# Kernel optimization log

Hardware: AMD Instinct MI355X
Metric: run time of the kernel (lower is better)

The kernel has to match this reference:

```python
import jax, jax.numpy as jnp
import numpy as np

IN_FEATS = 128
OUT_FEATS = 128
ASSIGN_DIM = 256
BATCH_SIZE = 8
N = 12288
E = 196608
CPG = ASSIGN_DIM // BATCH_SIZE  # clusters per graph (block width of the mask)


def setup_inputs() -> dict:
    key = jax.random.key(0)
    ks = jax.random.split(key, 6)
    x = jax.random.normal(ks[0], (N, IN_FEATS), dtype=jnp.float32)
    edge_index = jax.random.randint(ks[1], (2, E), 0, N, dtype=jnp.int32)
    batch = jnp.sort(jax.random.randint(ks[2], (N,), 0, BATCH_SIZE, dtype=jnp.int32))
    s = 1.0 / np.sqrt(2 * IN_FEATS)
    W_embd = jax.random.uniform(ks[3], (2 * IN_FEATS, OUT_FEATS), minval=-s, maxval=s, dtype=jnp.float32)
    b_embd = jnp.zeros((OUT_FEATS,), jnp.float32)
    W_pool = jax.random.uniform(ks[4], (2 * IN_FEATS, ASSIGN_DIM), minval=-s, maxval=s, dtype=jnp.float32)
    b_pool = jnp.zeros((ASSIGN_DIM,), jnp.float32)
    return dict(x=x, edge_index=edge_index, batch=batch,
                W_embd=W_embd, b_embd=b_embd, W_pool=W_pool, b_pool=b_pool)


def _sage_conv(x, src, dst, W, b):
    # GraphSAGE mean aggregator, concat([self, agg]) @ W + b, row L2-normalize.
    agg = jax.ops.segment_sum(x[src], dst, num_segments=N)                 # [N, F]
    deg = jax.ops.segment_sum(jnp.ones((E,), x.dtype), dst, num_segments=N)
    agg = agg / jnp.maximum(deg, 1.0)[:, None]
    h = jnp.concatenate([x, agg], axis=-1) @ W + b
    return h / jnp.maximum(jnp.linalg.norm(h, axis=-1, keepdims=True), 1e-12)


def _masked_softmax_nonme(m, mask):
    # memory_efficient=False branch of masked_softmax
    r = jax.nn.softmax(m * mask, axis=-1)
    r = r * mask
    return r / (r.sum(axis=-1, keepdims=True) + 1e-13)


def reference(x, edge_index, batch, W_embd, b_embd, W_pool, b_pool):
    src, dst = edge_index[0], edge_index[1]
    embed = _sage_conv(x, src, dst, W_embd, b_embd)    # [N, out_feats]
    pooled = _sage_conv(x, src, dst, W_pool, b_pool)   # [N, assign_dim]

    # block-diagonal mask: node i sees the assign columns of its own graph
    col_graph = jnp.arange(ASSIGN_DIM, dtype=batch.dtype) // CPG
    mask = (batch[:, None] == col_graph[None, :]).astype(pooled.dtype)  # [N, assign_dim]

    result = _masked_softmax_nonme(pooled, mask)        # [N, assign_dim]
    h = result.T @ embed                                # [assign_dim, out_feats]

    # adjacency coarsening: S^T A S with edge weights = 1 (duplicates sum)
    Ar = jax.ops.segment_sum(result[dst], src, num_segments=N)  # A @ result
    adj_new = result.T @ Ar                              # [assign_dim, assign_dim]

    # link prediction loss: ||A_dense - S S^T||_F / N^2 (dense NxN, as original)
    A_dense = jnp.zeros((N, N), result.dtype).at[src, dst].add(1.0)
    adj_loss = jnp.linalg.norm(A_dense - result @ result.T) / (N ** 2)

    # entropy loss over Categorical(probs=mask): uniform over each block
    p = mask / mask.sum(axis=-1, keepdims=True)
    ent = -jnp.sum(jnp.where(p > 0, p * jnp.log(jnp.where(p > 0, p, 1.0)), 0.0), axis=-1)
    entropy_loss = ent.sum()

    return adj_new, h, adj_loss, entropy_loss
```

## Files before the change

### kernel.cpp

```cpp
#include <hip/hip_runtime.h>
#include <math.h>

#define NN 12288
#define EE 196608
#define FIN 128
#define AD 256
#define NG 8
#define ACH 32
#define GCH 16
#define BCAP 64
#define APITCH 8256
#define HPITCH 4160
#define GPITCH 1088

using short8 = __attribute__((ext_vector_type(8))) short;
using floatx4 = __attribute__((ext_vector_type(4))) float;

__device__ __forceinline__ unsigned short f2bf(float f) {
  union { float f; unsigned u; } v; v.f = f;
  unsigned r = v.u + 0x7FFFu + ((v.u >> 16) & 1u);
  return (unsigned short)(r >> 16);
}


__global__ __launch_bounds__(256) void k_edgeB(const int* __restrict__ src, const int* __restrict__ dst,
    const int* __restrict__ batch,
    const float* __restrict__ We, const float* __restrict__ be,
    const float* __restrict__ Wp, const float* __restrict__ bp,
    unsigned* cnt_dst, unsigned* cnt_src, int* __restrict__ bdst, int* __restrict__ bsrc,
    unsigned short* __restrict__ WTb, float* __restrict__ bcat, int* __restrict__ gstart) {
  unsigned i = blockIdx.x * 256u + threadIdx.x;
  if (i < EE) {
    int s = src[i], d = dst[i];
    unsigned p = atomicAdd(&cnt_dst[d], 1u);
    if (p < BCAP) bdst[(size_t)d * BCAP + p] = s;
  } else if (i < 2u * EE) {
    unsigned e = i - EE;
    int s = src[e], d = dst[e];
    int gd = batch[d];
    unsigned q = atomicAdd(&cnt_src[s], 1u);
    if (q < BCAP) bsrc[(size_t)s * BCAP + q] = (gd << 14) | d;
  } else {
    unsigned j = i - 2u * EE;
    {
      unsigned n = j >> 8, k = j & 255u;
      float v = (n < 128u) ? We[k * 128u + n] : Wp[k * 256u + (n - 128u)];
      WTb[j] = f2bf(v);
    }
    if (j < 384u) bcat[j] = (j < 128u) ? be[j] : bp[j - 128u];
    if (j <= NG) {
      int g = (int)j, lo = 0, hi = NN;
      while (lo < hi) { int mid = (lo + hi) >> 1; if (batch[mid] < g) lo = mid + 1; else hi = mid; }
      gstart[g] = lo;
    }
  }
}


__global__ __launch_bounds__(256) void k_dupagg(const float* __restrict__ x,
    const unsigned* __restrict__ cnt_dst, const int* __restrict__ bdst,
    unsigned short* __restrict__ Zb, unsigned* __restrict__ dup_part) {
  int node = blockIdx.x * 4 + (threadIdx.x >> 6);
  int lane = threadIdx.x & 63;
  int h = lane >> 5, c = lane & 31;
  unsigned deg = cnt_dst[node];
  unsigned m = deg < BCAP ? deg : BCAP;
  const int* bk = bdst + (size_t)node * BCAP;
  const float4* x4 = (const float4*)x;

  int si = ((unsigned)lane < m) ? bk[lane] : -2;

  unsigned cnt = 0;
  for (unsigned j = 0; j < m; j++) {
    int sj = __shfl(si, (int)j, 64);
    cnt += (si == sj) ? 1u : 0u;
  }

  float4 a = {0.f, 0.f, 0.f, 0.f};
  for (unsigned e = (unsigned)h; e < m; e += 2) {
    int sj = __shfl(si, (int)e, 64);
    float4 v = x4[(size_t)sj * 32 + c];
    a.x += v.x; a.y += v.y; a.z += v.z; a.w += v.w;
  }

  a.x += __shfl_xor(a.x, 32, 64);
  a.y += __shfl_xor(a.y, 32, 64);
  a.z += __shfl_xor(a.z, 32, 64);
  a.w += __shfl_xor(a.w, 32, 64);

#pragma unroll
  for (int o = 32; o >= 1; o >>= 1) cnt += __shfl_xor(cnt, o, 64);
  if (lane == 0) dup_part[node] = cnt;

  float inv = 1.f / fmaxf((float)deg, 1.f);
  float4 sv = x4[(size_t)node * 32 + c];
  ushort4 o4;
  if (h == 0) {
    o4.x = f2bf(sv.x); o4.y = f2bf(sv.y); o4.z = f2bf(sv.z); o4.w = f2bf(sv.w);
  } else {
    o4.x = f2bf(a.x * inv); o4.y = f2bf(a.y * inv);
    o4.z = f2bf(a.z * inv); o4.w = f2bf(a.w * inv);
  }
  ((ushort4*)Zb)[(size_t)node * 64 + h * 32 + c] = o4;
}


__global__ __launch_bounds__(256) void k_gemmnorm(const unsigned short* __restrict__ Zb,
    const unsigned short* __restrict__ WTb, const float* __restrict__ bcat,
    const int* __restrict__ batch, float* __restrict__ embed, float* __restrict__ Rc) {
  __shared__ unsigned short Bl[24 * 512];
  __shared__ unsigned short Al[4 * 512];
  int t = threadIdx.x;
  int gm = blockIdx.x * 64;
  int w = t >> 6, l = t & 63;

  floatx4 acc[24] = {};

  for (int kc = 0; kc < 8; kc++) {
    __syncthreads();
#pragma unroll
    for (int i = 0; i < 7; i++) {
      int p = t + i * 256;
      if (p < 1536) {
        int n = p >> 2, quad = p & 3;
        uint4 v = *(const uint4*)&WTb[(size_t)n * 256 + kc * 32 + quad * 8];
        *(uint4*)&Bl[(n >> 4) * 512 + ((n & 15) + 16 * quad) * 8] = v;
      } else {
        int p2 = p - 1536;
        int m = p2 >> 2, quad = p2 & 3;
        uint4 v = *(const uint4*)&Zb[(size_t)(gm + m) * 256 + kc * 32 + quad * 8];
        *(uint4*)&Al[(m >> 4) * 512 + ((m & 15) + 16 * quad) * 8] = v;
      }
    }
    __syncthreads();
    short8 a = *(const short8*)&Al[w * 512 + l * 8];
#pragma unroll
    for (int tt = 0; tt < 24; tt++) {
      short8 b = *(const short8*)&Bl[tt * 512 + l * 8];
      acc[tt] = __builtin_amdgcn_mfma_f32_16x16x32_bf16(a, b, acc[tt], 0, 0, 0);
    }
  }

  int col16 = l & 15, quad = l >> 4;
#pragma unroll
  for (int tt = 0; tt < 24; tt++) {
    float b = bcat[tt * 16 + col16];
    acc[tt][0] += b; acc[tt][1] += b; acc[tt][2] += b; acc[tt][3] += b;
  }

#pragma unroll
  for (int r = 0; r < 4; r++) {
    int node = gm + w * 16 + quad * 4 + r;
    float ss = 0.f;
#pragma unroll
    for (int tt = 0; tt < 8; tt++) { float v = acc[tt][r]; ss += v * v; }
#pragma unroll
    for (int o = 8; o >= 1; o >>= 1) ss += __shfl_xor(ss, o, 64);
    float inv = 1.f / fmaxf(sqrtf(ss), 1e-12f);
#pragma unroll
    for (int tt = 0; tt < 8; tt++)
      embed[(size_t)node * 128 + tt * 16 + col16] = acc[tt][r] * inv;
    float ss2 = 0.f;
#pragma unroll
    for (int tt = 8; tt < 24; tt++) { float v = acc[tt][r]; ss2 += v * v; }
#pragma unroll
    for (int o = 8; o >= 1; o >>= 1) ss2 += __shfl_xor(ss2, o, 64);
    float inv2 = 1.f / fmaxf(sqrtf(ss2), 1e-12f);
    int g = batch[node];
    float v0 = 0.f, v1 = 0.f;
#pragma unroll
    for (int tg = 0; tg < 8; tg++) {
      bool sel = (tg == g);
      v0 = sel ? acc[8 + 2 * tg][r] : v0;
      v1 = sel ? acc[9 + 2 * tg][r] : v1;
    }
    v0 *= inv2; v1 *= inv2;
    float mx = fmaxf(v0, v1);
#pragma unroll
    for (int o = 8; o >= 1; o >>= 1) mx = fmaxf(mx, __shfl_xor(mx, o, 64));
    float e0 = expf(v0 - mx), e1 = expf(v1 - mx);
    float sm = e0 + e1;
#pragma unroll
    for (int o = 8; o >= 1; o >>= 1) sm += __shfl_xor(sm, o, 64);
    float rr = 1.f / sm;
    Rc[(size_t)node * 32 + col16] = e0 * rr;
    Rc[(size_t)node * 32 + 16 + col16] = e1 * rr;
  }
}


__global__ __launch_bounds__(256) void k_ar(const float* __restrict__ Rc,
    const unsigned* __restrict__ cnt_src, const int* __restrict__ bsrc,
    float* __restrict__ Ar) {
  int node = blockIdx.x * 4 + (threadIdx.x >> 6);
  int lane = threadIdx.x & 63;
  int lg = lane >> 3, li = lane & 7;
  unsigned deg = cnt_src[node];
  unsigned m = deg < BCAP ? deg : BCAP;
  const int* bk = bsrc + (size_t)node * BCAP;
  const float4* R4 = (const float4*)Rc;

  int pk = ((unsigned)lane < m) ? bk[lane] : (8 << 14);

  float4 acc[8] = {};
#pragma unroll 2
  for (unsigned k = 0; k < m; k += 8) {
    int packed = __shfl(pk, (int)(k + (unsigned)lg), 64);
    int d = packed & 16383, g = packed >> 14;
    float4 r = R4[(size_t)d * 8 + li];
#pragma unroll
    for (int j = 0; j < 8; j++) {
      float wj = (g == j) ? 1.f : 0.f;
      acc[j].x = fmaf(wj, r.x, acc[j].x);
      acc[j].y = fmaf(wj, r.y, acc[j].y);
      acc[j].z = fmaf(wj, r.z, acc[j].z);
      acc[j].w = fmaf(wj, r.w, acc[j].w);
    }
  }

#pragma unroll
  for (int j = 0; j < 8; j++) {
#pragma unroll
    for (int o = 8; o <= 32; o <<= 1) {
      acc[j].x += __shfl_xor(acc[j].x, o, 64);
      acc[j].y += __shfl_xor(acc[j].y, o, 64);
      acc[j].z += __shfl_xor(acc[j].z, o, 64);
      acc[j].w += __shfl_xor(acc[j].w, o, 64);
    }
  }
  float4 wv = acc[0];
#pragma unroll
  for (int j = 1; j < 8; j++) if (lg == j) wv = acc[j];
  ((float4*)Ar)[(size_t)node * 64 + lane] = wv;
}


__global__ __launch_bounds__(256) void k_big3(const float* __restrict__ Rc,
    const float* __restrict__ embed, const float* __restrict__ Ar, const int* __restrict__ gstart,
    float* __restrict__ part_h, float* __restrict__ part_adj, float* __restrict__ Gpart) {
  int role = blockIdx.z;
  int g = blockIdx.x, ch = blockIdx.y;
  if (role == 2 && ch >= GCH) return;
  int s0 = gstart[g], e0 = gstart[g + 1];
  int nch = (role == 2) ? GCH : ACH;
  int per = (e0 - s0 + nch - 1) / nch;
  int i0 = s0 + ch * per;
  int i1 = i0 + per; if (i1 > e0) i1 = e0;
  int t = threadIdx.x;
  __shared__ float rcs[128][32];

  if (role == 0) {
    int f4 = t & 31, c1g = t >> 5;
    float4 acc[4] = {};
    const float4* E4 = (const float4*)embed;
    for (int ib = i0; ib < i1; ib += 64) {
      int cnt = i1 - ib; if (cnt > 64) cnt = 64;
      __syncthreads();
      const float4* s4 = (const float4*)(Rc + (size_t)ib * 32);
      for (int idx = t; idx < cnt * 8; idx += 256) ((float4*)rcs)[idx] = s4[idx];
      __syncthreads();
      for (int n = 0; n < cnt; n++) {
        float4 e4 = E4[(size_t)(ib + n) * 32 + f4];
        float4 r = *(const float4*)&rcs[n][c1g * 4];
        float rv[4] = {r.x, r.y, r.z, r.w};
#pragma unroll
        for (int j = 0; j < 4; j++) {
          acc[j].x += rv[j] * e4.x; acc[j].y += rv[j] * e4.y;
          acc[j].z += rv[j] * e4.z; acc[j].w += rv[j] * e4.w;
        }
      }
    }
    float* p = part_h + (size_t)(g * ACH + ch) * HPITCH;
#pragma unroll
    for (int j = 0; j < 4; j++)
      *(float4*)&p[(c1g * 4 + j) * 128 + f4 * 4] = acc[j];
  } else if (role == 1) {
    int c2q = t & 63, c1g = t >> 6;
    float4 acc[8] = {};
    const float4* Ar4 = (const float4*)Ar;
    for (int ib = i0; ib < i1; ib += 64) {
      int cnt = i1 - ib; if (cnt > 64) cnt = 64;
      __syncthreads();
      const float4* s4 = (const float4*)(Rc + (size_t)ib * 32);
      for (int idx = t; idx < cnt * 8; idx += 256) ((float4*)rcs)[idx] = s4[idx];
      __syncthreads();
      for (int n = 0; n < cnt; n++) {
        float4 a4 = Ar4[(size_t)(ib + n) * 64 + c2q];
        float4 r0 = *(const float4*)&rcs[n][c1g * 8];
        float4 r1 = *(const float4*)&rcs[n][c1g * 8 + 4];
        float rv[8] = {r0.x, r0.y, r0.z, r0.w, r1.x, r1.y, r1.z, r1.w};
#pragma unroll
        for (int j = 0; j < 8; j++) {
          acc[j].x += rv[j] * a4.x; acc[j].y += rv[j] * a4.y;
          acc[j].z += rv[j] * a4.z; acc[j].w += rv[j] * a4.w;
        }
      }
    }
    float* p = part_adj + (size_t)(g * ACH + ch) * APITCH;
#pragma unroll
    for (int j = 0; j < 8; j++)
      *(float4*)&p[(c1g * 8 + j) * 256 + c2q * 4] = acc[j];
  } else {
    int c2q = t & 7, c1 = t >> 3;
    float4 acc = {};
    for (int ib = i0; ib < i1; ib += 128) {
      int cnt = i1 - ib; if (cnt > 128) cnt = 128;
      __syncthreads();
      const float4* s4 = (const float4*)(Rc + (size_t)ib * 32);
      for (int idx = t; idx < cnt * 8; idx += 256) ((float4*)rcs)[idx] = s4[idx];
      __syncthreads();
      for (int n = 0; n < cnt; n++) {
        float4 r2 = *(const float4*)&rcs[n][c2q * 4];
        float r1 = rcs[n][c1];
        acc.x += r1 * r2.x; acc.y += r1 * r2.y; acc.z += r1 * r2.z; acc.w += r1 * r2.w;
      }
    }
    *(float4*)&Gpart[(size_t)(g * GCH + ch) * GPITCH + c1 * 32 + c2q * 4] = acc;
  }
}


__global__ __launch_bounds__(256) void k_red3(const float* __restrict__ part_adj,
    const float* __restrict__ part_h, const float* __restrict__ Gpart,
    const unsigned* __restrict__ dup_part,
    float* __restrict__ outa, float* __restrict__ outh,
    double* __restrict__ acc, unsigned* __restrict__ done, float* __restrict__ out) {
  int b = blockIdx.x, t = threadIdx.x;
  int lane = t & 63;
  if (b < 256) {
    int i = b * 256 + t;
    int g = i >> 13, off = i & 8191;
    const float* base = part_adj + (size_t)g * ACH * APITCH + off;
    float s = 0.f;
#pragma unroll
    for (int ch = 0; ch < ACH; ch++) s += base[(size_t)ch * APITCH];
    outa[i] = s;
    if (t == b) atomicAdd(&acc[0], (double)s);
  } else if (b < 384) {
    int j = (b - 256) * 256 + t;
    int g = j >> 12, off = j & 4095;
    const float* base = part_h + (size_t)g * ACH * HPITCH + off;
    float s = 0.f;
#pragma unroll
    for (int ch = 0; ch < ACH; ch++) s += base[(size_t)ch * HPITCH];
    outh[j] = s;
  } else if (b < 416) {
    int j = (b - 384) * 256 + t;
    int g = j >> 10, off = j & 1023;
    const float* base = Gpart + (size_t)g * GCH * GPITCH + off;
    float s = 0.f;
#pragma unroll
    for (int ch = 0; ch < GCH; ch++) s += base[(size_t)ch * GPITCH];
    double g2 = (double)s * (double)s;
#pragma unroll
    for (int o = 32; o >= 1; o >>= 1) g2 += __shfl_xor(g2, o, 64);
    if (lane == 0) atomicAdd(&acc[1], g2);
  } else {
    int j = (b - 416) * 256 + t;
    double a2 = (double)dup_part[j];
#pragma unroll
    for (int o = 32; o >= 1; o >>= 1) a2 += __shfl_xor(a2, o, 64);
    if (lane == 0) atomicAdd(&acc[2], a2);
  }
  __syncthreads();
  if (t == 0) {
    unsigned prev = atomicAdd(done, 1u);
    if (prev == gridDim.x - 1) {
      double trf = atomicAdd(&acc[0], 0.0);
      double g2f = atomicAdd(&acc[1], 0.0);
      double a2f = atomicAdd(&acc[2], 0.0);
      double val = a2f - 2.0 * trf + g2f;
      if (val < 0.0) val = 0.0;
      out[98304] = (float)(sqrt(val) / ((double)NN * (double)NN));
      out[98305] = (float)((double)NN * log(32.0));
    }
  }
}


extern "C" void kernel_launch(void* const* d_in, const int* in_sizes, int n_in,
                              void* d_out, int out_size, void* d_ws, size_t ws_size,
                              hipStream_t stream) {
  const float* x = (const float*)d_in[0];
  const int* ei = (const int*)d_in[1];
  const int* src = ei;
  const int* dst = ei + EE;
  const int* batch = (const int*)d_in[2];
  const float* Wemb = (const float*)d_in[3];
  const float* bemb = (const float*)d_in[4];
  const float* Wpool = (const float*)d_in[5];
  const float* bpool = (const float*)d_in[6];
  float* out = (float*)d_out;

  char* w = (char*)d_ws;
  size_t off = 0;
  auto A = [&](size_t bytes) -> char* {
    char* p = w + off;
    off += (bytes + 255) & ~(size_t)255;
    return p;
  };
  unsigned* cnt_dst = (unsigned*)A(NN * 4);
  unsigned* cnt_src = (unsigned*)A(NN * 4);
  double* acc = (double*)A(3 * 8);
  unsigned* done = (unsigned*)A(4);
  size_t zero_bytes = off;
  int* bdst = (int*)A((size_t)NN * BCAP * 4);
  int* bsrc = (int*)A((size_t)NN * BCAP * 4);
  int* gstart = (int*)A(64);
  unsigned* dup_part = (unsigned*)A(NN * 4);
  unsigned short* Zb = (unsigned short*)A((size_t)NN * 256 * 2);
  float* embed = (float*)A((size_t)NN * FIN * 4);
  float* Rc = (float*)A((size_t)NN * 32 * 4);
  float* Ar = (float*)A((size_t)NN * AD * 4);
  unsigned short* WTb = (unsigned short*)A(384 * 256 * 2);
  float* bcat = (float*)A(384 * 4);
  float* part_h = (float*)A((size_t)8 * ACH * HPITCH * 4);
  float* part_adj = (float*)A((size_t)8 * ACH * APITCH * 4);
  float* Gpart = (float*)A((size_t)8 * GCH * GPITCH * 4);
  (void)ws_size; (void)in_sizes; (void)n_in; (void)out_size;

  hipMemsetAsync(d_ws, 0, zero_bytes, stream);
  k_edgeB<<<dim3(2 * EE / 256 + 384), dim3(256), 0, stream>>>(src, dst, batch,
      Wemb, bemb, Wpool, bpool, cnt_dst, cnt_src, bdst, bsrc, WTb, bcat, gstart);
  k_dupagg<<<dim3(NN / 4), dim3(256), 0, stream>>>(x, cnt_dst, bdst, Zb, dup_part);
  k_gemmnorm<<<dim3(NN / 64), dim3(256), 0, stream>>>(Zb, WTb, bcat, batch, embed, Rc);
  k_ar<<<dim3(NN / 4), dim3(256), 0, stream>>>(Rc, cnt_src, bsrc, Ar);
  k_big3<<<dim3(8, ACH, 3), dim3(256), 0, stream>>>(Rc, embed, Ar, gstart, part_h, part_adj, Gpart);
  k_red3<<<dim3(464), dim3(256), 0, stream>>>(part_adj, part_h, Gpart, dup_part,
      out, out + 65536, acc, done, out);
}
```

Measured before the change: 169.2 us.

## Fuse adjacency gather into coarsening GEMM and accumulate adj via atomics

The kernel that computes A@R into a global NxAD buffer is removed. Its per-node gather now runs inside the adj-coarsening role of the big kernel, with each block building Ar rows for 16 nodes in shared memory and consuming them right away. Partial adj tiles are float-atomically added straight into the output, which drops the part_adj buffer and its reduction. The trace now reads the diagonal from the finished output. This avoids writing and re-reading a 12 MB Ar buffer and one launch, at the cost of float atomics (nondeterministic summation order), an extra memset, and a gather that is serialized inside fewer blocks.

Result: slower. 226.5 us (+33.8%).

```diff
diff --git a/kernel.cpp b/kernel.cpp
--- a/kernel.cpp
+++ b/kernel.cpp
@@ -9,7 +9,6 @@
 #define ACH 32
 #define GCH 16
 #define BCAP 64
-#define APITCH 8256
 #define HPITCH 4160
 #define GPITCH 1088
 
@@ -189,69 +188,96 @@
 }
 
 
-__global__ __launch_bounds__(256) void k_ar(const float* __restrict__ Rc,
+__global__ __launch_bounds__(256) void k_bigF(const float* __restrict__ Rc,
+    const float* __restrict__ embed,
     const unsigned* __restrict__ cnt_src, const int* __restrict__ bsrc,
-    float* __restrict__ Ar) {
-  int node = blockIdx.x * 4 + (threadIdx.x >> 6);
-  int lane = threadIdx.x & 63;
-  int lg = lane >> 3, li = lane & 7;
-  unsigned deg = cnt_src[node];
-  unsigned m = deg < BCAP ? deg : BCAP;
-  const int* bk = bsrc + (size_t)node * BCAP;
-  const float4* R4 = (const float4*)Rc;
-
-  int pk = ((unsigned)lane < m) ? bk[lane] : (8 << 14);
-
-  float4 acc[8] = {};
-#pragma unroll 2
-  for (unsigned k = 0; k < m; k += 8) {
-    int packed = __shfl(pk, (int)(k + (unsigned)lg), 64);
-    int d = packed & 16383, g = packed >> 14;
-    float4 r = R4[(size_t)d * 8 + li];
-#pragma unroll
-    for (int j = 0; j < 8; j++) {
-      float wj = (g == j) ? 1.f : 0.f;
-      acc[j].x = fmaf(wj, r.x, acc[j].x);
-      acc[j].y = fmaf(wj, r.y, acc[j].y);
-      acc[j].z = fmaf(wj, r.z, acc[j].z);
-      acc[j].w = fmaf(wj, r.w, acc[j].w);
-    }
-  }
-
-#pragma unroll
-  for (int j = 0; j < 8; j++) {
-#pragma unroll
-    for (int o = 8; o <= 32; o <<= 1) {
-      acc[j].x += __shfl_xor(acc[j].x, o, 64);
-      acc[j].y += __shfl_xor(acc[j].y, o, 64);
-      acc[j].z += __shfl_xor(acc[j].z, o, 64);
-      acc[j].w += __shfl_xor(acc[j].w, o, 64);
-    }
-  }
-  float4 wv = acc[0];
-#pragma unroll
-  for (int j = 1; j < 8; j++) if (lg == j) wv = acc[j];
-  ((float4*)Ar)[(size_t)node * 64 + lane] = wv;
-}
-
-
-__global__ __launch_bounds__(256) void k_big3(const float* __restrict__ Rc,
-    const float* __restrict__ embed, const float* __restrict__ Ar, const int* __restrict__ gstart,
-    float* __restrict__ part_h, float* __restrict__ part_adj, float* __restrict__ Gpart) {
+    const int* __restrict__ gstart,
+    float* __restrict__ part_h, float* __restrict__ Gpart, float* __restrict__ outa) {
   int role = blockIdx.z;
   int g = blockIdx.x, ch = blockIdx.y;
-  if (role == 2 && ch >= GCH) return;
+  int t = threadIdx.x;
+  __shared__ __align__(16) char smem[18432];
   int s0 = gstart[g], e0 = gstart[g + 1];
-  int nch = (role == 2) ? GCH : ACH;
-  int per = (e0 - s0 + nch - 1) / nch;
-  int i0 = s0 + ch * per;
-  int i1 = i0 + per; if (i1 > e0) i1 = e0;
-  int t = threadIdx.x;
-  __shared__ float rcs[128][32];
-
-  if (role == 0) {
+
+  if (role == 1) {
+    int per = (e0 - s0 + 63) >> 6;
+    int i0 = s0 + ch * per;
+    int i1 = i0 + per; if (i1 > e0) i1 = e0;
+    int w = t >> 6, lane = t & 63;
+    int lg = lane >> 3, li = lane & 7;
+    int c1g = t >> 6, c2q = t & 63;
+    float4* ar_s = (float4*)smem;
+    float* rc_s = (float*)(smem + 16384);
+    const float4* R4 = (const float4*)Rc;
+    float4 racc[8] = {};
+    for (int ib = i0; ib < i1; ib += 16) {
+      int cnt = i1 - ib; if (cnt > 16) cnt = 16;
+      __syncthreads();
+      for (int idx = t; idx < cnt * 8; idx += 256)
+        ((float4*)rc_s)[idx] = R4[(size_t)ib * 8 + idx];
+      for (int nl = w; nl < cnt; nl += 4) {
+        int node = ib + nl;
+        unsigned deg = cnt_src[node];
+        unsigned m = deg < BCAP ? deg : BCAP;
+        const int* bk = bsrc + (size_t)node * BCAP;
+        int pk = ((unsigned)lane < m) ? bk[lane] : (8 << 14);
+        float4 a8[8] = {};
+        for (unsigned k = 0; k < m; k += 8) {
+          int packed = __shfl(pk, (int)(k + (unsigned)lg), 64);
+          int d = packed & 16383, gg = packed >> 14;
+          float4 r = R4[(size_t)d * 8 + li];
+#pragma unroll
+          for (int j = 0; j < 8; j++) {
+            float wj = (gg == j) ? 1.f : 0.f;
+            a8[j].x = fmaf(wj, r.x, a8[j].x);
+            a8[j].y = fmaf(wj, r.y, a8[j].y);
+            a8[j].z = fmaf(wj, r.z, a8[j].z);
+            a8[j].w = fmaf(wj, r.w, a8[j].w);
+          }
+        }
+#pragma unroll
+        for (int j = 0; j < 8; j++) {
+#pragma unroll
+          for (int o = 8; o <= 32; o <<= 1) {
+            a8[j].x += __shfl_xor(a8[j].x, o, 64);
+            a8[j].y += __shfl_xor(a8[j].y, o, 64);
+            a8[j].z += __shfl_xor(a8[j].z, o, 64);
+            a8[j].w += __shfl_xor(a8[j].w, o, 64);
+          }
+        }
+        float4 wv = a8[0];
+#pragma unroll
+        for (int j = 1; j < 8; j++) if (lg == j) wv = a8[j];
+        ar_s[nl * 64 + lane] = wv;
+      }
+      __syncthreads();
+      for (int n = 0; n < cnt; n++) {
+        float4 a4 = ar_s[n * 64 + c2q];
+        const float* rr = &rc_s[n * 32 + c1g * 8];
+#pragma unroll
+        for (int j = 0; j < 8; j++) {
+          float rv = rr[j];
+          racc[j].x += rv * a4.x; racc[j].y += rv * a4.y;
+          racc[j].z += rv * a4.z; racc[j].w += rv * a4.w;
+        }
+      }
+    }
+#pragma unroll
+    for (int j = 0; j < 8; j++) {
+      float* dp = &outa[(size_t)(g * 32 + c1g * 8 + j) * 256 + c2q * 4];
+      atomicAdd(dp + 0, racc[j].x);
+      atomicAdd(dp + 1, racc[j].y);
+      atomicAdd(dp + 2, racc[j].z);
+      atomicAdd(dp + 3, racc[j].w);
+    }
+  } else if (role == 0) {
+    if (ch >= ACH) return;
+    int per = (e0 - s0 + ACH - 1) / ACH;
+    int i0 = s0 + ch * per;
+    int i1 = i0 + per; if (i1 > e0) i1 = e0;
+    float (*rcs)[32] = (float(*)[32])smem;
     int f4 = t & 31, c1g = t >> 5;
-    float4 acc[4] = {};
+    float4 hacc[4] = {};
     const float4* E4 = (const float4*)embed;
     for (int ib = i0; ib < i1; ib += 64) {
       int cnt = i1 - ib; if (cnt > 64) cnt = 64;
@@ -265,44 +291,23 @@
         float rv[4] = {r.x, r.y, r.z, r.w};
 #pragma unroll
         for (int j = 0; j < 4; j++) {
-          acc[j].x += rv[j] * e4.x; acc[j].y += rv[j] * e4.y;
-          acc[j].z += rv[j] * e4.z; acc[j].w += rv[j] * e4.w;
+          hacc[j].x += rv[j] * e4.x; hacc[j].y += rv[j] * e4.y;
+          hacc[j].z += rv[j] * e4.z; hacc[j].w += rv[j] * e4.w;
         }
       }
     }
     float* p = part_h + (size_t)(g * ACH + ch) * HPITCH;
 #pragma unroll
     for (int j = 0; j < 4; j++)
-      *(float4*)&p[(c1g * 4 + j) * 128 + f4 * 4] = acc[j];
-  } else if (role == 1) {
-    int c2q = t & 63, c1g = t >> 6;
-    float4 acc[8] = {};
-    const float4* Ar4 = (const float4*)Ar;
-    for (int ib = i0; ib < i1; ib += 64) {
-      int cnt = i1 - ib; if (cnt > 64) cnt = 64;
-      __syncthreads();
-      const float4* s4 = (const float4*)(Rc + (size_t)ib * 32);
-      for (int idx = t; idx < cnt * 8; idx += 256) ((float4*)rcs)[idx] = s4[idx];
-      __syncthreads();
-      for (int n = 0; n < cnt; n++) {
-        float4 a4 = Ar4[(size_t)(ib + n) * 64 + c2q];
-        float4 r0 = *(const float4*)&rcs[n][c1g * 8];
-        float4 r1 = *(const float4*)&rcs[n][c1g * 8 + 4];
-        float rv[8] = {r0.x, r0.y, r0.z, r0.w, r1.x, r1.y, r1.z, r1.w};
-#pragma unroll
-        for (int j = 0; j < 8; j++) {
-          acc[j].x += rv[j] * a4.x; acc[j].y += rv[j] * a4.y;
-          acc[j].z += rv[j] * a4.z; acc[j].w += rv[j] * a4.w;
-        }
-      }
-    }
-    float* p = part_adj + (size_t)(g * ACH + ch) * APITCH;
-#pragma unroll
-    for (int j = 0; j < 8; j++)
-      *(float4*)&p[(c1g * 8 + j) * 256 + c2q * 4] = acc[j];
+      *(float4*)&p[(c1g * 4 + j) * 128 + f4 * 4] = hacc[j];
   } else {
+    if (ch >= GCH) return;
+    int per = (e0 - s0 + GCH - 1) / GCH;
+    int i0 = s0 + ch * per;
+    int i1 = i0 + per; if (i1 > e0) i1 = e0;
+    float (*rcs)[32] = (float(*)[32])smem;
     int c2q = t & 7, c1 = t >> 3;
-    float4 acc = {};
+    float4 gacc = {};
     for (int ib = i0; ib < i1; ib += 128) {
       int cnt = i1 - ib; if (cnt > 128) cnt = 128;
       __syncthreads();
@@ -312,40 +317,35 @@
       for (int n = 0; n < cnt; n++) {
         float4 r2 = *(const float4*)&rcs[n][c2q * 4];
         float r1 = rcs[n][c1];
-        acc.x += r1 * r2.x; acc.y += r1 * r2.y; acc.z += r1 * r2.z; acc.w += r1 * r2.w;
+        gacc.x += r1 * r2.x; gacc.y += r1 * r2.y; gacc.z += r1 * r2.z; gacc.w += r1 * r2.w;
       }
     }
-    *(float4*)&Gpart[(size_t)(g * GCH + ch) * GPITCH + c1 * 32 + c2q * 4] = acc;
-  }
-}
-
-
-__global__ __launch_bounds__(256) void k_red3(const float* __restrict__ part_adj,
-    const float* __restrict__ part_h, const float* __restrict__ Gpart,
-    const unsigned* __restrict__ dup_part,
-    float* __restrict__ outa, float* __restrict__ outh,
+    *(float4*)&Gpart[(size_t)(g * GCH + ch) * GPITCH + c1 * 32 + c2q * 4] = gacc;
+  }
+}
+
+
+__global__ __launch_bounds__(256) void k_red3(const float* __restrict__ part_h,
+    const float* __restrict__ Gpart, const unsigned* __restrict__ dup_part,
+    const float* __restrict__ outa, float* __restrict__ outh,
     double* __restrict__ acc, unsigned* __restrict__ done, float* __restrict__ out) {
   int b = blockIdx.x, t = threadIdx.x;
   int lane = t & 63;
-  if (b < 256) {
-    int i = b * 256 + t;
-    int g = i >> 13, off = i & 8191;
-    const float* base = part_adj + (size_t)g * ACH * APITCH + off;
-    float s = 0.f;
-#pragma unroll
-    for (int ch = 0; ch < ACH; ch++) s += base[(size_t)ch * APITCH];
-    outa[i] = s;
-    if (t == b) atomicAdd(&acc[0], (double)s);
-  } else if (b < 384) {
-    int j = (b - 256) * 256 + t;
+  if (b == 0) {
+    double s = (double)outa[t * 257];
+#pragma unroll
+    for (int o = 32; o >= 1; o >>= 1) s += __shfl_xor(s, o, 64);
+    if (lane == 0) atomicAdd(&acc[0], s);
+  } else if (b < 129) {
+    int j = (b - 1) * 256 + t;
     int g = j >> 12, off = j & 4095;
     const float* base = part_h + (size_t)g * ACH * HPITCH + off;
     float s = 0.f;
 #pragma unroll
     for (int ch = 0; ch < ACH; ch++) s += base[(size_t)ch * HPITCH];
     outh[j] = s;
-  } else if (b < 416) {
-    int j = (b - 384) * 256 + t;
+  } else if (b < 161) {
+    int j = (b - 129) * 256 + t;
     int g = j >> 10, off = j & 1023;
     const float* base = Gpart + (size_t)g * GCH * GPITCH + off;
     float s = 0.f;
@@ -356,7 +356,7 @@
     for (int o = 32; o >= 1; o >>= 1) g2 += __shfl_xor(g2, o, 64);
     if (lane == 0) atomicAdd(&acc[1], g2);
   } else {
-    int j = (b - 416) * 256 + t;
+    int j = (b - 161) * 256 + t;
     double a2 = (double)dup_part[j];
 #pragma unroll
     for (int o = 32; o >= 1; o >>= 1) a2 += __shfl_xor(a2, o, 64);
@@ -411,21 +411,21 @@
   unsigned short* Zb = (unsigned short*)A((size_t)NN * 256 * 2);
   float* embed = (float*)A((size_t)NN * FIN * 4);
   float* Rc = (float*)A((size_t)NN * 32 * 4);
-  float* Ar = (float*)A((size_t)NN * AD * 4);
   unsigned short* WTb = (unsigned short*)A(384 * 256 * 2);
   float* bcat = (float*)A(384 * 4);
   float* part_h = (float*)A((size_t)8 * ACH * HPITCH * 4);
-  float* part_adj = (float*)A((size_t)8 * ACH * APITCH * 4);
   float* Gpart = (float*)A((size_t)8 * GCH * GPITCH * 4);
   (void)ws_size; (void)in_sizes; (void)n_in; (void)out_size;
 
   hipMemsetAsync(d_ws, 0, zero_bytes, stream);
+  hipMemsetAsync(out, 0, 65536 * 4, stream);
+
   k_edgeB<<<dim3(2 * EE / 256 + 384), dim3(256), 0, stream>>>(src, dst, batch,
       Wemb, bemb, Wpool, bpool, cnt_dst, cnt_src, bdst, bsrc, WTb, bcat, gstart);
   k_dupagg<<<dim3(NN / 4), dim3(256), 0, stream>>>(x, cnt_dst, bdst, Zb, dup_part);
   k_gemmnorm<<<dim3(NN / 64), dim3(256), 0, stream>>>(Zb, WTb, bcat, batch, embed, Rc);
-  k_ar<<<dim3(NN / 4), dim3(256), 0, stream>>>(Rc, cnt_src, bsrc, Ar);
-  k_big3<<<dim3(8, ACH, 3), dim3(256), 0, stream>>>(Rc, embed, Ar, gstart, part_h, part_adj, Gpart);
-  k_red3<<<dim3(464), dim3(256), 0, stream>>>(part_adj, part_h, Gpart, dup_part,
+  k_bigF<<<dim3(8, 64, 3), dim3(256), 0, stream>>>(Rc, embed, cnt_src, bsrc, gstart,
+      part_h, Gpart, out);
+  k_red3<<<dim3(209), dim3(256), 0, stream>>>(part_h, Gpart, dup_part,
       out, out + 65536, acc, done, out);
 }
```
